# Kernel optimization log

Measured on AMD Instinct MI355X. Metric: run time of the kernel, lower is better.

The kernel has to match this reference:

```python
import jax, jax.numpy as jnp
import numpy as np

N, C, G, H = 64, 23, 20000, 64  # batch, NB_CHROM, NB_GENES, HIDDEN


def setup_inputs() -> dict:
    key = jax.random.key(0)
    k1, k2, k3 = jax.random.split(key, 3)
    x = jax.random.normal(k1, (N, G, H), dtype=jnp.float32)
    # each gene belongs to exactly one chromosome -> one-hot composition matrix (C, G)
    assign = jax.random.randint(k2, (G,), 0, C)
    chrom_mat = jax.nn.one_hot(assign, C, dtype=jnp.float32).T  # (C, G)
    attention = jax.random.normal(k3, (C, H), dtype=jnp.float32)
    return {"x": x, "chrom_mat": chrom_mat, "attention": attention}


def reference(x, chrom_mat, attention):
    # Original: h = einsum('ij,njk->nijk', mask, x); att = einsum('ij,kijm->kim', A, h.transpose(2,3))
    # Algebraically identical fused form: att[n,i,g] = mask[i,g] * <A[i,:], x[n,g,:]>
    att = jnp.einsum('ih,ngh->nig', attention, x) * chrom_mat[None]  # (N, C, G)
    mask = (att != 0).astype(att.dtype)  # mask = att.bool().byte()
    att = jnp.exp(jax.nn.leaky_relu(att, negative_slope=0.2)) * mask
    att = att / jnp.maximum(att.sum(axis=2, keepdims=True), jnp.float32(1e-10))
    return jnp.einsum('nig,ngh->nih', att, x)  # bmm(att, x) -> (N, C, H)
```

## Files before the change

kernel.cpp:

```cpp
#include <hip/hip_runtime.h>
#include <hip/hip_bf16.h>

#define N_ 64
#define C_ 23
#define G_ 20000
#define H_ 64
#define S_ 4

template <int CTRL>
__device__ __forceinline__ float ror_add(float v) {
    int r = __builtin_amdgcn_update_dpp(0, __float_as_int(v), CTRL, 0xf, 0xf, true);
    return v + __int_as_float(r);
}

__global__ void assign_kernel(const float* __restrict__ chrom,
                              int* __restrict__ assign,
                              int* __restrict__ counts) {
    int g = blockIdx.x * blockDim.x + threadIdx.x;
    if (g >= G_) return;
    int c_found = 0;
    #pragma unroll
    for (int c = 0; c < C_; ++c) {
        if (chrom[c * G_ + g] != 0.f) c_found = c;
    }
    assign[g] = c_found;
    atomicAdd(&counts[c_found], 1);
}

__global__ void scan_kernel(const int* __restrict__ counts,
                            int* __restrict__ offsets,
                            int* __restrict__ cursors) {
    if (threadIdx.x == 0 && blockIdx.x == 0) {
        int run = 0;
        for (int c = 0; c < C_; ++c) {
            offsets[c] = run;
            cursors[c] = run;
            run += counts[c];
        }
        offsets[C_] = run;
    }
}

__global__ void scatter_kernel(const int* __restrict__ assign,
                               int* __restrict__ cursors,
                               int* __restrict__ sorted_g) {
    int g = blockIdx.x * blockDim.x + threadIdx.x;
    if (g >= G_) return;
    int c = assign[g];
    int pos = atomicAdd(&cursors[c], 1);
    sorted_g[pos] = g;
}

__global__ __launch_bounds__(256) void main_pass(
    const float* __restrict__ x,
    const float* __restrict__ attn,
    const int* __restrict__ offsets,
    const int* __restrict__ sorted_g,
    float* __restrict__ acc,
    float* __restrict__ denom)
{
    int b = blockIdx.x;
    int s = b % S_; b /= S_;
    int c = b % C_; b /= C_;
    int n = b;

    int beg = offsets[c];
    int end = offsets[c + 1];
    int cnt = end - beg;
    int L   = (cnt + S_ - 1) / S_;
    int lo  = beg + s * L;
    int hi  = min(beg + (s + 1) * L, end);

    int tid = threadIdx.x;
    int sub = tid & 15;
    int grp = tid >> 4;

    const float4 a4 = ((const float4*)(attn + c * H_))[sub];

    float4 accv = make_float4(0.f, 0.f, 0.f, 0.f);
    float dsum = 0.f;

    const float* xb = x + (size_t)n * G_ * H_;

    #pragma unroll 2
    for (int p = lo + grp; p < hi; p += 16) {
        int g = sorted_g[p];
        const float4 x4 = ((const float4*)(xb + (size_t)g * H_))[sub];
        float part = fmaf(a4.x, x4.x, fmaf(a4.y, x4.y, fmaf(a4.z, x4.z, a4.w * x4.w)));
        part = ror_add<0x128>(part);
        part = ror_add<0x124>(part);
        part = ror_add<0x122>(part);
        part = ror_add<0x121>(part);
        float w = 0.f;
        if (part != 0.f) {
            float lr = (part >= 0.f) ? part : 0.2f * part;
            w = __expf(lr);
        }
        accv.x = fmaf(w, x4.x, accv.x);
        accv.y = fmaf(w, x4.y, accv.y);
        accv.z = fmaf(w, x4.z, accv.z);
        accv.w = fmaf(w, x4.w, accv.w);
        dsum += w;
    }

    #pragma unroll
    for (int m = 16; m <= 32; m <<= 1) {
        accv.x += __shfl_xor(accv.x, m);
        accv.y += __shfl_xor(accv.y, m);
        accv.z += __shfl_xor(accv.z, m);
        accv.w += __shfl_xor(accv.w, m);
        dsum   += __shfl_xor(dsum, m);
    }

    int lane = tid & 63;
    float* accp = acc + ((size_t)n * C_ + c) * H_;
    if (lane < 16) {
        atomicAdd(accp + sub * 4 + 0, accv.x);
        atomicAdd(accp + sub * 4 + 1, accv.y);
        atomicAdd(accp + sub * 4 + 2, accv.z);
        atomicAdd(accp + sub * 4 + 3, accv.w);
        if (sub == 0) atomicAdd(denom + n * C_ + c, dsum);
    }
}

__global__ void finalize_kernel(const float* __restrict__ acc,
                                const float* __restrict__ denom,
                                float* __restrict__ out) {
    int i = blockIdx.x * blockDim.x + threadIdx.x;
    if (i >= N_ * C_ * H_) return;
    int nc = i >> 6;
    float d = fmaxf(denom[nc], 1e-10f);
    out[i] = acc[i] / d;
}

extern "C" void kernel_launch(void* const* d_in, const int* in_sizes, int n_in,
                              void* d_out, int out_size, void* d_ws, size_t ws_size,
                              hipStream_t stream) {
    const float* x     = (const float*)d_in[0];
    const float* chrom = (const float*)d_in[1];
    const float* attn  = (const float*)d_in[2];
    float* out = (float*)d_out;

    float* acc    = (float*)d_ws;
    float* denom  = acc + (size_t)N_ * C_ * H_;
    int*   counts  = (int*)(denom + (size_t)N_ * C_);
    int*   cursors = counts + C_;
    int*   offsets = cursors + C_;
    int*   assign  = offsets + (C_ + 1);
    int*   sorted  = assign + G_;

    size_t zero_bytes = ((size_t)N_ * C_ * H_ + (size_t)N_ * C_ + C_) * sizeof(float);
    hipMemsetAsync(d_ws, 0, zero_bytes, stream);

    int gb = (G_ + 255) / 256;
    assign_kernel<<<gb, 256, 0, stream>>>(chrom, assign, counts);
    scan_kernel<<<1, 64, 0, stream>>>(counts, offsets, cursors);
    scatter_kernel<<<gb, 256, 0, stream>>>(assign, cursors, sorted);

    main_pass<<<N_ * C_ * S_, 256, 0, stream>>>(x, attn, offsets, sorted, acc, denom);

    finalize_kernel<<<(N_ * C_ * H_ + 255) / 256, 256, 0, stream>>>(acc, denom, out);
}
```

Measured before the change: 533.0 us.

## Fuse bucketing into one kernel and drop split-reduction atomics and finalize pass

Replaces the assign/scan/scatter pipeline with a single kernel that writes each gene into a per-chromosome bucket of capacity G, indexed by an atomic counter. The main pass no longer splits each (n,c) across four blocks. It reduces the four waves through shared memory and writes the normalized output directly, which removes the global atomics, the large workspace memset and the finalize kernel. The aim is fewer launches and less synchronization, at the cost of a quarter as many blocks (1472) and therefore less parallelism per (n,c). The unroll factor goes from 2 to 4 to compensate.

After: 498.3 us. 6.5% less time.

```diff
diff --git a/kernel.cpp b/kernel.cpp
--- a/kernel.cpp
+++ b/kernel.cpp
@@ -1,11 +1,9 @@
 #include <hip/hip_runtime.h>
-#include <hip/hip_bf16.h>
 
 #define N_ 64
 #define C_ 23
 #define G_ 20000
 #define H_ 64
-#define S_ 4
 
 template <int CTRL>
 __device__ __forceinline__ float ror_add(float v) {
@@ -13,9 +11,9 @@
     return v + __int_as_float(r);
 }
 
-__global__ void assign_kernel(const float* __restrict__ chrom,
-                              int* __restrict__ assign,
-                              int* __restrict__ counts) {
+__global__ void bucket_kernel(const float* __restrict__ chrom,
+                              int* __restrict__ counts,
+                              int* __restrict__ bucket) {
     int g = blockIdx.x * blockDim.x + threadIdx.x;
     if (g >= G_) return;
     int c_found = 0;
@@ -23,57 +21,28 @@
     for (int c = 0; c < C_; ++c) {
         if (chrom[c * G_ + g] != 0.f) c_found = c;
     }
-    assign[g] = c_found;
-    atomicAdd(&counts[c_found], 1);
-}
-
-__global__ void scan_kernel(const int* __restrict__ counts,
-                            int* __restrict__ offsets,
-                            int* __restrict__ cursors) {
-    if (threadIdx.x == 0 && blockIdx.x == 0) {
-        int run = 0;
-        for (int c = 0; c < C_; ++c) {
-            offsets[c] = run;
-            cursors[c] = run;
-            run += counts[c];
-        }
-        offsets[C_] = run;
-    }
-}
-
-__global__ void scatter_kernel(const int* __restrict__ assign,
-                               int* __restrict__ cursors,
-                               int* __restrict__ sorted_g) {
-    int g = blockIdx.x * blockDim.x + threadIdx.x;
-    if (g >= G_) return;
-    int c = assign[g];
-    int pos = atomicAdd(&cursors[c], 1);
-    sorted_g[pos] = g;
+    int pos = atomicAdd(&counts[c_found], 1);
+    bucket[c_found * G_ + pos] = g;
 }
 
 __global__ __launch_bounds__(256) void main_pass(
     const float* __restrict__ x,
     const float* __restrict__ attn,
-    const int* __restrict__ offsets,
-    const int* __restrict__ sorted_g,
-    float* __restrict__ acc,
-    float* __restrict__ denom)
+    const int* __restrict__ counts,
+    const int* __restrict__ bucket,
+    float* __restrict__ out)
 {
     int b = blockIdx.x;
-    int s = b % S_; b /= S_;
-    int c = b % C_; b /= C_;
-    int n = b;
+    int c = b % C_;
+    int n = b / C_;
 
-    int beg = offsets[c];
-    int end = offsets[c + 1];
-    int cnt = end - beg;
-    int L   = (cnt + S_ - 1) / S_;
-    int lo  = beg + s * L;
-    int hi  = min(beg + (s + 1) * L, end);
+    int cnt = counts[c];
+    const int* __restrict__ bk = bucket + c * G_;
 
-    int tid = threadIdx.x;
-    int sub = tid & 15;
-    int grp = tid >> 4;
+    int tid  = threadIdx.x;
+    int sub  = tid & 15;
+    int gid  = tid >> 4;
+    int wave = tid >> 6;
 
     const float4 a4 = ((const float4*)(attn + c * H_))[sub];
 
@@ -82,9 +51,9 @@
 
     const float* xb = x + (size_t)n * G_ * H_;
 
-    #pragma unroll 2
-    for (int p = lo + grp; p < hi; p += 16) {
-        int g = sorted_g[p];
+    #pragma unroll 4
+    for (int p = gid; p < cnt; p += 16) {
+        int g = bk[p];
         const float4 x4 = ((const float4*)(xb + (size_t)g * H_))[sub];
         float part = fmaf(a4.x, x4.x, fmaf(a4.y, x4.y, fmaf(a4.z, x4.z, a4.w * x4.w)));
         part = ror_add<0x128>(part);
@@ -112,25 +81,24 @@
         dsum   += __shfl_xor(dsum, m);
     }
 
+    __shared__ float4 pacc[4][16];
+    __shared__ float  pd[4];
     int lane = tid & 63;
-    float* accp = acc + ((size_t)n * C_ + c) * H_;
     if (lane < 16) {
-        atomicAdd(accp + sub * 4 + 0, accv.x);
-        atomicAdd(accp + sub * 4 + 1, accv.y);
-        atomicAdd(accp + sub * 4 + 2, accv.z);
-        atomicAdd(accp + sub * 4 + 3, accv.w);
-        if (sub == 0) atomicAdd(denom + n * C_ + c, dsum);
+        pacc[wave][lane] = accv;
+        if (lane == 0) pd[wave] = dsum;
     }
-}
-
-__global__ void finalize_kernel(const float* __restrict__ acc,
-                                const float* __restrict__ denom,
-                                float* __restrict__ out) {
-    int i = blockIdx.x * blockDim.x + threadIdx.x;
-    if (i >= N_ * C_ * H_) return;
-    int nc = i >> 6;
-    float d = fmaxf(denom[nc], 1e-10f);
-    out[i] = acc[i] / d;
+    __syncthreads();
+    if (tid < 16) {
+        float4 s0 = pacc[0][tid], s1 = pacc[1][tid], s2 = pacc[2][tid], s3 = pacc[3][tid];
+        float d = fmaxf(pd[0] + pd[1] + pd[2] + pd[3], 1e-10f);
+        float4 o;
+        o.x = (s0.x + s1.x + s2.x + s3.x) / d;
+        o.y = (s0.y + s1.y + s2.y + s3.y) / d;
+        o.z = (s0.z + s1.z + s2.z + s3.z) / d;
+        o.w = (s0.w + s1.w + s2.w + s3.w) / d;
+        ((float4*)(out + ((size_t)(n * C_ + c)) * H_))[tid] = o;
+    }
 }
 
 extern "C" void kernel_launch(void* const* d_in, const int* in_sizes, int n_in,
@@ -141,23 +109,13 @@
     const float* attn  = (const float*)d_in[2];
     float* out = (float*)d_out;
 
-    float* acc    = (float*)d_ws;
-    float* denom  = acc + (size_t)N_ * C_ * H_;
-    int*   counts  = (int*)(denom + (size_t)N_ * C_);
-    int*   cursors = counts + C_;
-    int*   offsets = cursors + C_;
-    int*   assign  = offsets + (C_ + 1);
-    int*   sorted  = assign + G_;
+    int* counts = (int*)d_ws;
+    int* bucket = counts + C_;
 
-    size_t zero_bytes = ((size_t)N_ * C_ * H_ + (size_t)N_ * C_ + C_) * sizeof(float);
-    hipMemsetAsync(d_ws, 0, zero_bytes, stream);
+    hipMemsetAsync(counts, 0, C_ * sizeof(int), stream);
 
     int gb = (G_ + 255) / 256;
-    assign_kernel<<<gb, 256, 0, stream>>>(chrom, assign, counts);
-    scan_kernel<<<1, 64, 0, stream>>>(counts, offsets, cursors);
-    scatter_kernel<<<gb, 256, 0, stream>>>(assign, cursors, sorted);
+    bucket_kernel<<<gb, 256, 0, stream>>>(chrom, counts, bucket);
 
-    main_pass<<<N_ * C_ * S_, 256, 0, stream>>>(x, attn, offsets, sorted, acc, denom);
-
-    finalize_kernel<<<(N_ * C_ * H_ + 255) / 256, 256, 0, stream>>>(acc, denom, out);
+    main_pass<<<N_ * C_, 256, 0, stream>>>(x, attn, counts, bucket, out);
 }
```
